# Optimization experiments

Hardware: AMD Instinct MI355X
Metric: run time of the kernel (lower is better)

The kernel has to match this reference:

```python
import jax, jax.numpy as jnp
import numpy as np


def setup_inputs() -> dict:
    key = jax.random.key(0)
    inputs = jax.random.normal(key, (8, 384, 1248, 4), dtype=jnp.float32)
    return {"inputs": inputs, "focal": 3}


def reference(inputs, focal):
    # cardinal_fod = last-dim - 1; outputs have 2^cardinal_fod channels.
    cardinal_fod = inputs.shape[-1] - 1
    n_sets = 2 ** cardinal_fod
    # Channel j (j = 0 .. n_sets-1). Channel 0 is the initial zeros column;
    # for j >= 1: bel[..., j] = 1 if (j & focal) == focal else 0,
    #             pl[...,  j] = 1 if (j & focal) >  0    else 0.
    # j = 0 satisfies neither condition (focal > 0), so one vectorized mask
    # covers all channels.
    j = jnp.arange(n_sets, dtype=jnp.int32)
    contain = jnp.bitwise_and(j, jnp.int32(focal))
    bel_mask = (contain == jnp.int32(focal)).astype(inputs.dtype)  # [n_sets]
    pl_mask = (contain > 0).astype(inputs.dtype)                   # [n_sets]
    out_shape = inputs.shape[:-1] + (n_sets,)  # [B, 384, 1248, n_sets]
    bel = jnp.broadcast_to(bel_mask, out_shape)
    pl = jnp.broadcast_to(pl_mask, out_shape)
    return (bel, pl)
```

## Files before the change

kernel.cpp:

```cpp
#include <hip/hip_runtime.h>


__global__ void __launch_bounds__(256)
BeliefPlausibilityFocused_35656818492191_kernel(const int* __restrict__ focal_p,
                                                float* __restrict__ out,
                                                long long n4_per_out) {
    const int focal = *focal_p;
    long long i = (long long)blockIdx.x * blockDim.x + threadIdx.x;
    if (i >= n4_per_out) return;

    const int c0 = ((int)i & 1) * 4;
    float b[4], p[4];
#pragma unroll
    for (int k = 0; k < 4; ++k) {
        const int j = c0 + k;
        const int c = j & focal;
        b[k] = (c == focal) ? 1.0f : 0.0f;
        p[k] = (c > 0) ? 1.0f : 0.0f;
    }

    float4* __restrict__ out_bel = (float4*)out;
    float4* __restrict__ out_pl  = (float4*)(out + 4 * n4_per_out);
    out_bel[i] = make_float4(b[0], b[1], b[2], b[3]);
    out_pl[i]  = make_float4(p[0], p[1], p[2], p[3]);
}

extern "C" void kernel_launch(void* const* d_in, const int* in_sizes, int n_in,
                              void* d_out, int out_size, void* d_ws, size_t ws_size,
                              hipStream_t stream) {
    const int* focal = (const int*)d_in[1];
    float* out = (float*)d_out;

    const long long per_out = (long long)out_size / 2;
    const long long n4 = per_out / 4;

    const int threads = 256;
    const int blocks = (int)((n4 + threads - 1) / threads);
    BeliefPlausibilityFocused_35656818492191_kernel<<<blocks, threads, 0, stream>>>(
        focal, out, n4);
}
```

Before: 262.7 us.

## Use grid-stride loop with nontemporal float4 stores covering both outputs

Replaces the one-thread-per-float4 launch with a grid capped at 2048 blocks. Each thread walks the combined bel+pl buffer, writing four consecutive float4 per iteration through nontemporal stores, with the mask values computed once per thread. The goal is to cut launch and block-scheduling overhead and avoid cache pollution on this pure-write workload. The cost is that each store instruction now has lanes 64 bytes apart rather than contiguous, which may hurt write coalescing.

```diff
diff --git a/kernel.cpp b/kernel.cpp
--- a/kernel.cpp
+++ b/kernel.cpp
@@ -1,28 +1,47 @@
 #include <hip/hip_runtime.h>
 
+
+typedef float f32x4 __attribute__((ext_vector_type(4)));
 
 __global__ void __launch_bounds__(256)
 BeliefPlausibilityFocused_35656818492191_kernel(const int* __restrict__ focal_p,
                                                 float* __restrict__ out,
-                                                long long n4_per_out) {
+                                                long long n4_per_out,
+                                                long long n4_total) {
     const int focal = *focal_p;
-    long long i = (long long)blockIdx.x * blockDim.x + threadIdx.x;
-    if (i >= n4_per_out) return;
 
-    const int c0 = ((int)i & 1) * 4;
-    float b[4], p[4];
+    float b[8], p[8];
 #pragma unroll
-    for (int k = 0; k < 4; ++k) {
-        const int j = c0 + k;
+    for (int j = 0; j < 8; ++j) {
         const int c = j & focal;
-        b[k] = (c == focal) ? 1.0f : 0.0f;
-        p[k] = (c > 0) ? 1.0f : 0.0f;
+        b[j] = (c == focal) ? 1.0f : 0.0f;
+        p[j] = (c > 0) ? 1.0f : 0.0f;
     }
+    const f32x4 bA = {b[0], b[1], b[2], b[3]};
+    const f32x4 bB = {b[4], b[5], b[6], b[7]};
+    const f32x4 pA = {p[0], p[1], p[2], p[3]};
+    const f32x4 pB = {p[4], p[5], p[6], p[7]};
 
-    float4* __restrict__ out_bel = (float4*)out;
-    float4* __restrict__ out_pl  = (float4*)(out + 4 * n4_per_out);
-    out_bel[i] = make_float4(b[0], b[1], b[2], b[3]);
-    out_pl[i]  = make_float4(p[0], p[1], p[2], p[3]);
+    f32x4* __restrict__ o = (f32x4*)out;
+
+    const long long stride = (long long)gridDim.x * blockDim.x * 4;
+    long long i4 = ((long long)blockIdx.x * blockDim.x + threadIdx.x) * 4;
+
+    for (; i4 + 3 < n4_total; i4 += stride) {
+#pragma unroll
+        for (int k = 0; k < 4; ++k) {
+            const long long idx = i4 + k;
+            const bool is_pl = (idx >= n4_per_out);
+            const f32x4 v = (k & 1) ? (is_pl ? pB : bB) : (is_pl ? pA : bA);
+            __builtin_nontemporal_store(v, o + idx);
+        }
+    }
+    for (; i4 < n4_total; ++i4) {
+        const bool is_pl = (i4 >= n4_per_out);
+        const bool odd = (i4 & 1);
+        const f32x4 v = odd ? (is_pl ? pB : bB) : (is_pl ? pA : bA);
+        __builtin_nontemporal_store(v, o + i4);
+    }
 }
 
 extern "C" void kernel_launch(void* const* d_in, const int* in_sizes, int n_in,
@@ -32,10 +51,13 @@
     float* out = (float*)d_out;
 
     const long long per_out = (long long)out_size / 2;
-    const long long n4 = per_out / 4;
+    const long long n4_per_out = per_out / 4;
+    const long long n4_total = (long long)out_size / 4;
 
     const int threads = 256;
-    const int blocks = (int)((n4 + threads - 1) / threads);
+    long long want = (n4_total + 4LL * threads - 1) / (4LL * threads);
+    const int blocks = (int)((want < 2048) ? want : 2048);
+
     BeliefPlausibilityFocused_35656818492191_kernel<<<blocks, threads, 0, stream>>>(
-        focal, out, n4);
+        focal, out, n4_per_out, n4_total);
 }
```

New measurement: 487.5 us. 85.5% more time.
